# Optimization experiments

Measured on AMD Instinct MI355X. Metric: run time of the kernel, lower is better.

The kernel has to match this reference:

```python
import jax, jax.numpy as jnp
import numpy as np

B, T, C = 4, 2048, 1024
H = 16
D = C // H  # head_dim = 64

def setup_inputs() -> dict:
    key = jax.random.key(0)
    k1, k2, k3 = jax.random.split(key, 3)
    x = jax.random.normal(k1, (B, T, C), dtype=jnp.float32)
    w_qkv = jax.random.normal(k2, (C, 3 * C), dtype=jnp.float32) * (1.0 / np.sqrt(C))
    w_proj = jax.random.normal(k3, (C, C), dtype=jnp.float32) * (1.0 / np.sqrt(C))
    return {"x": x, "w_qkv": w_qkv, "w_proj": w_proj}

def reference(x, w_qkv, w_proj):
    Bq, Tq, Cq = x.shape
    qkv = x @ w_qkv                                   # [B,T,3C]
    q, k, v = jnp.split(qkv, 3, axis=2)
    # [B,T,C] -> [B,H,T,D]
    q = q.reshape(Bq, Tq, H, D).transpose(0, 2, 1, 3)
    k = k.reshape(Bq, Tq, H, D).transpose(0, 2, 1, 3)
    v = v.reshape(Bq, Tq, H, D).transpose(0, 2, 1, 3)
    att = jnp.einsum('bhqd,bhkd->bhqk', q, k) / jnp.sqrt(jnp.float32(D))
    causal = jnp.tril(jnp.ones((Tq, Tq), dtype=bool))
    att = jnp.where(causal[None, None], att, jnp.float32(-jnp.inf))
    att = jax.nn.softmax(att, axis=-1)
    y = jnp.einsum('bhqk,bhkd->bhqd', att, v)         # [B,H,T,D]
    y = y.transpose(0, 2, 1, 3).reshape(Bq, Tq, Cq)
    return y @ w_proj
```

## Files before the change

kernel.cpp:

```cpp
#include <hip/hip_runtime.h>

typedef unsigned short u16;
typedef __attribute__((ext_vector_type(8))) short s16x8;
typedef __attribute__((ext_vector_type(4))) float f32x4;
typedef __attribute__((ext_vector_type(16))) float f32x16;

#define MFMA(a, b, c) __builtin_amdgcn_mfma_f32_16x16x32_bf16((a), (b), (c), 0, 0, 0)
#define MFMA32(a, b, c) __builtin_amdgcn_mfma_f32_32x32x16_bf16((a), (b), (c), 0, 0, 0)

#define LDS16(gp, lp)                                                          \
  __builtin_amdgcn_global_load_lds(                                            \
      (__attribute__((address_space(1))) void*)(gp),                           \
      (__attribute__((address_space(3))) void*)(lp), 16, 0, 0)

#if __has_builtin(__builtin_amdgcn_exp2f)
#define EXP2F(x) __builtin_amdgcn_exp2f(x)
#else
#define EXP2F(x) exp2f(x)
#endif
#if __has_builtin(__builtin_amdgcn_rcpf)
#define RCPF(x) __builtin_amdgcn_rcpf(x)
#else
#define RCPF(x) (1.0f / (x))
#endif

__device__ __forceinline__ u16 f2bf(float f) {
  unsigned u = __float_as_uint(f);
  u += 0x7fffu + ((u >> 16) & 1u);
  return (u16)(u >> 16);
}

__device__ __forceinline__ int cvtpk(float a, float b) {
  int r;
  asm("v_cvt_pk_bf16_f32 %0, %1, %2" : "=v"(r) : "v"(a), "v"(b));
  return r;
}

__global__ void cast_x_kernel(const float* __restrict__ in, u16* __restrict__ out) {
  const int idx = (blockIdx.x * 256 + threadIdx.x) * 4;
  const float4 v = *(const float4*)(in + idx);
  ushort4 o;
  o.x = f2bf(v.x); o.y = f2bf(v.y); o.z = f2bf(v.z); o.w = f2bf(v.w);
  *(ushort4*)(out + idx) = o;
}

__global__ void transpose_cast(const float* __restrict__ in, u16* __restrict__ out,
                               int Kd, int Nd) {
  __shared__ float t[64][65];
  const int tid = threadIdx.x;
  const int nb = blockIdx.x * 64, kb = blockIdx.y * 64;
#pragma unroll
  for (int it = 0; it < 4; it++) {
    const int flat = it * 1024 + tid * 4;
    const int rr = flat >> 6, cc = flat & 63;
    const float4 v = *(const float4*)(in + (size_t)(kb + rr) * Nd + nb + cc);
    t[rr][cc] = v.x; t[rr][cc + 1] = v.y; t[rr][cc + 2] = v.z; t[rr][cc + 3] = v.w;
  }
  __syncthreads();
#pragma unroll
  for (int it = 0; it < 4; it++) {
    const int flat = it * 1024 + tid * 4;
    const int rn = flat >> 6, ck = flat & 63;
    ushort4 o;
    o.x = f2bf(t[ck][rn]);     o.y = f2bf(t[ck + 1][rn]);
    o.z = f2bf(t[ck + 2][rn]); o.w = f2bf(t[ck + 3][rn]);
    *(ushort4*)(out + (size_t)(nb + rn) * Kd + kb + ck) = o;
  }
}

template <int EPI>
__global__ __launch_bounds__(256, 2)
void gemm128(const u16* __restrict__ A, const u16* __restrict__ Bt,
             float* __restrict__ Cout, int Ndim,
             u16* __restrict__ qp, u16* __restrict__ kp, u16* __restrict__ vp) {
  __shared__ alignas(16) u16 As[128 * 32];
  __shared__ alignas(16) u16 Bs[128 * 32];
  const int tid = threadIdx.x;
  const int wave = tid >> 6, lane = tid & 63;
  const int r = lane & 15, qq = lane >> 4;
  const int wm = (wave >> 1) * 64, wn = (wave & 1) * 64;
  const int tn = blockIdx.x * 128, tm = blockIdx.y * 128;

  f32x4 acc[4][4];
#pragma unroll
  for (int i = 0; i < 4; i++)
#pragma unroll
    for (int j = 0; j < 4; j++) acc[i][j] = (f32x4){0.f, 0.f, 0.f, 0.f};

  const int c0 = tid, c1 = tid + 256;
  const u16* ga0 = A + (size_t)(tm + (c0 >> 2)) * 1024 + (c0 & 3) * 8;
  const u16* ga1 = A + (size_t)(tm + (c1 >> 2)) * 1024 + (c1 & 3) * 8;
  const u16* gb0 = Bt + (size_t)(tn + (c0 >> 2)) * 1024 + (c0 & 3) * 8;
  const u16* gb1 = Bt + (size_t)(tn + (c1 >> 2)) * 1024 + (c1 & 3) * 8;
  u16* la0 = As + c0 * 8; u16* la1 = As + c1 * 8;
  u16* lb0 = Bs + c0 * 8; u16* lb1 = Bs + c1 * 8;

  for (int k0 = 0; k0 < 1024; k0 += 32) {
    LDS16(ga0 + k0, la0);
    LDS16(ga1 + k0, la1);
    LDS16(gb0 + k0, lb0);
    LDS16(gb1 + k0, lb1);
    __syncthreads();
    s16x8 af[4], bfr[4];
#pragma unroll
    for (int f = 0; f < 4; f++)
      af[f] = *(const s16x8*)(As + (wm + f * 16 + r) * 32 + qq * 8);
#pragma unroll
    for (int f = 0; f < 4; f++)
      bfr[f] = *(const s16x8*)(Bs + (wn + f * 16 + r) * 32 + qq * 8);
#pragma unroll
    for (int fm = 0; fm < 4; fm++)
#pragma unroll
      for (int fn = 0; fn < 4; fn++)
        acc[fm][fn] = MFMA(af[fm], bfr[fn], acc[fm][fn]);
    __syncthreads();
  }

  if (EPI == 0) {
#pragma unroll
    for (int fm = 0; fm < 4; fm++) {
#pragma unroll
      for (int j2 = 0; j2 < 4; j2++) {
        const int mm = tm + wm + fm * 16 + qq * 4 + j2;
        const int bb = mm >> 11, tt = mm & 2047;
#pragma unroll
        for (int fn = 0; fn < 4; fn++) {
          const int n = tn + wn + fn * 16 + r;
          const u16 bv = f2bf(acc[fm][fn][j2]);
          const int which = n >> 10;
          const int hh = (n >> 6) & 15, dd = n & 63;
          const int bhh = bb * 16 + hh;
          if (which == 0)      qp[((size_t)bhh * 2048 + tt) * 64 + dd] = bv;
          else if (which == 1) kp[((size_t)bhh * 2048 + tt) * 64 + dd] = bv;
          else                 vp[((size_t)bhh * 64 + dd) * 2048 + tt] = bv;
        }
      }
    }
  } else {
#pragma unroll
    for (int fm = 0; fm < 4; fm++) {
#pragma unroll
      for (int j2 = 0; j2 < 4; j2++) {
        const int mm = tm + wm + fm * 16 + qq * 4 + j2;
#pragma unroll
        for (int fn = 0; fn < 4; fn++) {
          const int n = tn + wn + fn * 16 + r;
          Cout[(size_t)mm * Ndim + n] = acc[fm][fn][j2];
        }
      }
    }
  }
}

__global__ __launch_bounds__(256, 2)
void attn_fwd(const u16* __restrict__ qg, const u16* __restrict__ kg,
              const u16* __restrict__ vtg, u16* __restrict__ yg) {
  __shared__ alignas(16) u16 Kl[2][64 * 64];
  __shared__ alignas(16) u16 Vl[2][64 * 64];
  const int tid = threadIdx.x;
  const int w = tid >> 6, lane = tid & 63;
  const int q5 = lane & 31, hi = lane >> 5;
  const int qb = blockIdx.x * 128;
  const int bh = blockIdx.y;
  const int qrow = qb + w * 32 + q5;
  const float C = 0.18033688011112042f;

  const u16* qbase = qg + ((size_t)bh * 2048 + qrow) * 64;
  s16x8 qf[4];
#pragma unroll
  for (int ks = 0; ks < 4; ks++)
    qf[ks] = *(const s16x8*)(qbase + ks * 16 + hi * 8);

  const int c0 = tid, c1 = tid + 256;
  const int r0 = c0 >> 3, s0 = (c0 & 7) ^ (r0 & 7);
  const int r1 = c1 >> 3, s1 = (c1 & 7) ^ (r1 & 7);
  const u16* kga = kg + ((size_t)bh * 2048 + r0) * 64 + s0 * 8;
  const u16* kgb = kg + ((size_t)bh * 2048 + r1) * 64 + s1 * 8;
  const u16* vga = vtg + ((size_t)bh * 64 + r0) * 2048 + s0 * 8;
  const u16* vgb = vtg + ((size_t)bh * 64 + r1) * 2048 + s1 * 8;

  f32x16 ya, yb;
#pragma unroll
  for (int r = 0; r < 16; r++) { ya[r] = 0.f; yb[r] = 0.f; }
  float m_run = -3.0e38f, l_run = 0.f;

  const int nt = qb / 64 + 2;

#define STAGE(b, t)                                               \
  do {                                                            \
    LDS16(kga + (size_t)(t) * 4096, Kl[b] + c0 * 8);              \
    LDS16(kgb + (size_t)(t) * 4096, Kl[b] + c1 * 8);              \
    LDS16(vga + (size_t)(t) * 64,   Vl[b] + c0 * 8);              \
    LDS16(vgb + (size_t)(t) * 64,   Vl[b] + c1 * 8);              \
  } while (0)

  STAGE(0, 0);
  __syncthreads();

  for (int t = 0; t < nt; t++) {
    const int buf = t & 1;
    if (t + 1 < nt) STAGE(buf ^ 1, t + 1);
    const int kv0 = t * 64;
    const u16* Kb = Kl[buf];
    const u16* Vb = Vl[buf];

    if (kv0 <= qb + w * 32 + 31) {
      f32x16 sa, sb;
#pragma unroll
      for (int r = 0; r < 16; r++) { sa[r] = 0.f; sb[r] = 0.f; }
#pragma unroll
      for (int ks = 0; ks < 4; ks++) {
        const int slot = ((ks * 2 + hi) ^ (lane & 7)) * 8;
        const s16x8 ka  = *(const s16x8*)(Kb + q5 * 64 + slot);
        const s16x8 kb2 = *(const s16x8*)(Kb + (32 + q5) * 64 + slot);
        sa = MFMA32(ka, qf[ks], sa);
        sb = MFMA32(kb2, qf[ks], sb);
      }

      if (kv0 + 63 > qb + w * 32) {
#pragma unroll
        for (int r = 0; r < 16; r++) {
          const int kl = kv0 + (r & 3) + 8 * (r >> 2) + 4 * hi;
          if (kl > qrow)      sa[r] = -3.0e38f;
          if (kl + 32 > qrow) sb[r] = -3.0e38f;
        }
      }

      float mx = -3.0e38f;
#pragma unroll
      for (int r = 0; r < 16; r++) mx = fmaxf(mx, fmaxf(sa[r], sb[r]));
      mx = fmaxf(mx, __shfl_xor(mx, 32));
      const float m2 = fmaxf(m_run, mx * C);
      const float alpha = EXP2F(m_run - m2);
      m_run = m2;
      const float nm2 = -m2;
      float ls = 0.f;
#pragma unroll
      for (int r = 0; r < 16; r++) {
        const float p0 = EXP2F(fmaf(sa[r], C, nm2));
        const float p1 = EXP2F(fmaf(sb[r], C, nm2));
        sa[r] = p0; sb[r] = p1;
        ls += p0 + p1;
      }
      ls += __shfl_xor(ls, 32);
      l_run = l_run * alpha + ls;
#pragma unroll
      for (int r = 0; r < 16; r++) { ya[r] *= alpha; yb[r] *= alpha; }

      s16x8 bfrag[4];
#pragma unroll
      for (int kb = 0; kb < 2; kb++) {
        const f32x16* pv = kb ? &sb : &sa;
        int wv[8], xv[8];
#pragma unroll
        for (int i = 0; i < 8; i++) wv[i] = cvtpk((*pv)[2 * i], (*pv)[2 * i + 1]);
#pragma unroll
        for (int i = 0; i < 8; i++) xv[i] = __shfl_xor(wv[i], 32);
        union { int4 i4; s16x8 s8; } u0, u1;
        u0.i4 = hi ? make_int4(xv[2], xv[3], wv[2], wv[3])
                   : make_int4(wv[0], wv[1], xv[0], xv[1]);
        u1.i4 = hi ? make_int4(xv[6], xv[7], wv[6], wv[7])
                   : make_int4(wv[4], wv[5], xv[4], xv[5]);
        bfrag[kb * 2]     = u0.s8;
        bfrag[kb * 2 + 1] = u1.s8;
      }

#pragma unroll
      for (int ks4 = 0; ks4 < 4; ks4++) {
        const int sv = ((ks4 * 2 + hi) ^ (lane & 7)) * 8;
        const s16x8 va  = *(const s16x8*)(Vb + q5 * 64 + sv);
        const s16x8 vb2 = *(const s16x8*)(Vb + (32 + q5) * 64 + sv);
        ya = MFMA32(va, bfrag[ks4], ya);
        yb = MFMA32(vb2, bfrag[ks4], yb);
      }
    }
    __syncthreads();
  }
#undef STAGE

  const float linv = RCPF(l_run);
  const int b = bh >> 4, h = bh & 15;
  u16* yrow = yg + ((size_t)b * 2048 + qrow) * 1024 + h * 64;
#pragma unroll
  for (int dt = 0; dt < 2; dt++) {
    const f32x16* Y = dt ? &yb : &ya;
#pragma unroll
    for (int p2 = 0; p2 < 8; p2++) {
      const int pk = cvtpk((*Y)[2 * p2] * linv, (*Y)[2 * p2 + 1] * linv);
      const int d0 = dt * 32 + (p2 >> 1) * 8 + hi * 4 + (p2 & 1) * 2;
      *reinterpret_cast<int*>(yrow + d0) = pk;
    }
  }
}

extern "C" void kernel_launch(void* const* d_in, const int* in_sizes, int n_in,
                              void* d_out, int out_size, void* d_ws, size_t ws_size,
                              hipStream_t stream) {
  const float* x = (const float*)d_in[0];
  const float* wqkv = (const float*)d_in[1];
  const float* wproj = (const float*)d_in[2];
  float* out = (float*)d_out;

  char* ws = (char*)d_ws;
  u16* xb     = (u16*)(ws);
  u16* wqkvT  = (u16*)(ws + 16777216);
  u16* wprojT = (u16*)(ws + 23068672);
  u16* qw     = (u16*)(ws + 25165824);
  u16* kw     = (u16*)(ws + 41943040);
  u16* vtw    = (u16*)(ws + 58720256);
  u16* yw     = (u16*)(ws + 75497472);
  (void)in_sizes; (void)n_in; (void)out_size; (void)ws_size;

  cast_x_kernel<<<8192, 256, 0, stream>>>(x, xb);
  transpose_cast<<<dim3(48, 16), 256, 0, stream>>>(wqkv, wqkvT, 1024, 3072);
  transpose_cast<<<dim3(16, 16), 256, 0, stream>>>(wproj, wprojT, 1024, 1024);
  gemm128<0><<<dim3(24, 64), 256, 0, stream>>>(xb, wqkvT, nullptr, 3072, qw, kw, vtw);
  attn_fwd<<<dim3(16, 64), 256, 0, stream>>>(qw, kw, vtw, yw);
  gemm128<1><<<dim3(8, 64), 256, 0, stream>>>(yw, wprojT, out, 1024,
                                              nullptr, nullptr, nullptr);
}
```

Measured before the change: 317.3 us.

## Swizzle GEMM tiles, reorder attention blocks, lazy rescale, and MFMA priority hints

The GEMM remaps block IDs with an XCD-style swizzle so neighbouring tiles share an L2, and raises wave priority around the MFMA loops. The attention kernel launches heaviest (late) query blocks first and hoists the V fragment loads ahead of the softmax. It also skips the running-max rescale unless the max grows by more than a threshold, and splits the max and sum reductions into independent chains. Together these aim at L2 locality, causal load imbalance, and softmax latency, at the cost of small added precision risk from the lazy rescale and higher register use.

```diff
diff --git a/kernel.cpp b/kernel.cpp
--- a/kernel.cpp
+++ b/kernel.cpp
@@ -79,7 +79,11 @@
   const int wave = tid >> 6, lane = tid & 63;
   const int r = lane & 15, qq = lane >> 4;
   const int wm = (wave >> 1) * 64, wn = (wave & 1) * 64;
-  const int tn = blockIdx.x * 128, tm = blockIdx.y * 128;
+  const int gx = gridDim.x;
+  const int nwg = gx * gridDim.y;
+  const int bid = blockIdx.x + gx * blockIdx.y;
+  const int swz = (bid & 7) * (nwg >> 3) + (bid >> 3);
+  const int tn = (swz % gx) * 128, tm = (swz / gx) * 128;
 
   f32x4 acc[4][4];
 #pragma unroll
@@ -108,11 +112,13 @@
 #pragma unroll
     for (int f = 0; f < 4; f++)
       bfr[f] = *(const s16x8*)(Bs + (wn + f * 16 + r) * 32 + qq * 8);
+    __builtin_amdgcn_s_setprio(1);
 #pragma unroll
     for (int fm = 0; fm < 4; fm++)
 #pragma unroll
       for (int fn = 0; fn < 4; fn++)
         acc[fm][fn] = MFMA(af[fm], bfr[fn], acc[fm][fn]);
+    __builtin_amdgcn_s_setprio(0);
     __syncthreads();
   }
 
@@ -160,8 +166,9 @@
   const int tid = threadIdx.x;
   const int w = tid >> 6, lane = tid & 63;
   const int q5 = lane & 31, hi = lane >> 5;
-  const int qb = blockIdx.x * 128;
-  const int bh = blockIdx.y;
+  const int bh = blockIdx.x;
+  const int qi = (int)(gridDim.y - 1 - blockIdx.y);
+  const int qb = qi * 128;
   const int qrow = qb + w * 32 + q5;
   const float C = 0.18033688011112042f;
 
@@ -208,6 +215,7 @@
       f32x16 sa, sb;
 #pragma unroll
       for (int r = 0; r < 16; r++) { sa[r] = 0.f; sb[r] = 0.f; }
+      __builtin_amdgcn_s_setprio(1);
 #pragma unroll
       for (int ks = 0; ks < 4; ks++) {
         const int slot = ((ks * 2 + hi) ^ (lane & 7)) * 8;
@@ -216,6 +224,15 @@
         sa = MFMA32(ka, qf[ks], sa);
         sb = MFMA32(kb2, qf[ks], sb);
       }
+      __builtin_amdgcn_s_setprio(0);
+
+      s16x8 va[4], vb2[4];
+#pragma unroll
+      for (int ks4 = 0; ks4 < 4; ks4++) {
+        const int sv = ((ks4 * 2 + hi) ^ (lane & 7)) * 8;
+        va[ks4]  = *(const s16x8*)(Vb + q5 * 64 + sv);
+        vb2[ks4] = *(const s16x8*)(Vb + (32 + q5) * 64 + sv);
+      }
 
       if (kv0 + 63 > qb + w * 32) {
 #pragma unroll
@@ -226,26 +243,44 @@
         }
       }
 
-      float mx = -3.0e38f;
-#pragma unroll
-      for (int r = 0; r < 16; r++) mx = fmaxf(mx, fmaxf(sa[r], sb[r]));
+      float mx0 = -3.0e38f, mx1 = -3.0e38f, mx2 = -3.0e38f, mx3 = -3.0e38f;
+#pragma unroll
+      for (int r = 0; r < 16; r += 4) {
+        mx0 = fmaxf(mx0, fmaxf(sa[r], sb[r]));
+        mx1 = fmaxf(mx1, fmaxf(sa[r + 1], sb[r + 1]));
+        mx2 = fmaxf(mx2, fmaxf(sa[r + 2], sb[r + 2]));
+        mx3 = fmaxf(mx3, fmaxf(sa[r + 3], sb[r + 3]));
+      }
+      float mx = fmaxf(fmaxf(mx0, mx1), fmaxf(mx2, mx3));
       mx = fmaxf(mx, __shfl_xor(mx, 32));
-      const float m2 = fmaxf(m_run, mx * C);
-      const float alpha = EXP2F(m_run - m2);
-      m_run = m2;
-      const float nm2 = -m2;
-      float ls = 0.f;
-#pragma unroll
-      for (int r = 0; r < 16; r++) {
-        const float p0 = EXP2F(fmaf(sa[r], C, nm2));
-        const float p1 = EXP2F(fmaf(sb[r], C, nm2));
-        sa[r] = p0; sb[r] = p1;
-        ls += p0 + p1;
-      }
+      const float mxs = mx * C;
+
+      if (!__all(mxs - m_run <= 8.0f)) {
+        const float m2 = fmaxf(m_run, mxs);
+        const float alpha = EXP2F(m_run - m2);
+        m_run = m2;
+        l_run *= alpha;
+#pragma unroll
+        for (int r = 0; r < 16; r++) { ya[r] *= alpha; yb[r] *= alpha; }
+      }
+
+      const float nm2 = -m_run;
+      float ls0 = 0.f, ls1 = 0.f, ls2 = 0.f, ls3 = 0.f;
+#pragma unroll
+      for (int r = 0; r < 16; r += 4) {
+        float p;
+        p = EXP2F(fmaf(sa[r], C, nm2));     sa[r] = p;     ls0 += p;
+        p = EXP2F(fmaf(sa[r + 1], C, nm2)); sa[r + 1] = p; ls1 += p;
+        p = EXP2F(fmaf(sa[r + 2], C, nm2)); sa[r + 2] = p; ls2 += p;
+        p = EXP2F(fmaf(sa[r + 3], C, nm2)); sa[r + 3] = p; ls3 += p;
+        p = EXP2F(fmaf(sb[r], C, nm2));     sb[r] = p;     ls0 += p;
+        p = EXP2F(fmaf(sb[r + 1], C, nm2)); sb[r + 1] = p; ls1 += p;
+        p = EXP2F(fmaf(sb[r + 2], C, nm2)); sb[r + 2] = p; ls2 += p;
+        p = EXP2F(fmaf(sb[r + 3], C, nm2)); sb[r + 3] = p; ls3 += p;
+      }
+      float ls = (ls0 + ls1) + (ls2 + ls3);
       ls += __shfl_xor(ls, 32);
-      l_run = l_run * alpha + ls;
-#pragma unroll
-      for (int r = 0; r < 16; r++) { ya[r] *= alpha; yb[r] *= alpha; }
+      l_run += ls;
 
       s16x8 bfrag[4];
 #pragma unroll
@@ -265,14 +300,13 @@
         bfrag[kb * 2 + 1] = u1.s8;
       }
 
+      __builtin_amdgcn_s_setprio(1);
 #pragma unroll
       for (int ks4 = 0; ks4 < 4; ks4++) {
-        const int sv = ((ks4 * 2 + hi) ^ (lane & 7)) * 8;
-        const s16x8 va  = *(const s16x8*)(Vb + q5 * 64 + sv);
-        const s16x8 vb2 = *(const s16x8*)(Vb + (32 + q5) * 64 + sv);
-        ya = MFMA32(va, bfrag[ks4], ya);
-        yb = MFMA32(vb2, bfrag[ks4], yb);
-      }
+        ya = MFMA32(va[ks4], bfrag[ks4], ya);
+        yb = MFMA32(vb2[ks4], bfrag[ks4], yb);
+      }
+      __builtin_amdgcn_s_setprio(0);
     }
     __syncthreads();
   }
@@ -315,7 +349,7 @@
   transpose_cast<<<dim3(48, 16), 256, 0, stream>>>(wqkv, wqkvT, 1024, 3072);
   transpose_cast<<<dim3(16, 16), 256, 0, stream>>>(wproj, wprojT, 1024, 1024);
   gemm128<0><<<dim3(24, 64), 256, 0, stream>>>(xb, wqkvT, nullptr, 3072, qw, kw, vtw);
-  attn_fwd<<<dim3(16, 64), 256, 0, stream>>>(qw, kw, vtw, yw);
+  attn_fwd<<<dim3(64, 16), 256, 0, stream>>>(qw, kw, vtw, yw);
   gemm128<1><<<dim3(8, 64), 256, 0, stream>>>(yw, wprojT, out, 1024,
                                               nullptr, nullptr, nullptr);
 }
```

After: 269.8 us. -15.0%, faster.
